# Optimization experiments

Hardware: AMD Instinct MI355X
Metric: run time of the kernel (lower is better)

Reference implementation:

```python
import jax, jax.numpy as jnp
import numpy as np

E, D_IN, H, D_OUT = 8, 6, 32, 2
B = 1048576

def setup_inputs() -> dict:
    key = jax.random.key(0)
    ks = jax.random.split(key, 11)
    s = lambda *sh: 1.0 / np.sqrt(sh[-2])  # glorot-ish scale
    x = jax.random.normal(ks[0], (B, D_IN), dtype=jnp.float32)
    # stacked expert weights
    W1 = jax.random.normal(ks[1], (E, D_IN, H), dtype=jnp.float32) * (1.0/np.sqrt(D_IN))
    b1 = jnp.zeros((E, H), dtype=jnp.float32)
    W2 = jax.random.normal(ks[2], (E, H, H), dtype=jnp.float32) * (1.0/np.sqrt(H))
    b2 = jnp.zeros((E, H), dtype=jnp.float32)
    W3 = jax.random.normal(ks[3], (E, H, D_OUT), dtype=jnp.float32) * (1.0/np.sqrt(H))
    b3 = jnp.zeros((E, D_OUT), dtype=jnp.float32)
    # gating network
    Wg1 = jax.random.normal(ks[4], (D_IN, H), dtype=jnp.float32) * (1.0/np.sqrt(D_IN))
    bg1 = jnp.zeros((H,), dtype=jnp.float32)
    Wg2 = jax.random.normal(ks[5], (H, E), dtype=jnp.float32) * (1.0/np.sqrt(H))
    bg2 = jnp.zeros((E,), dtype=jnp.float32)
    return {"x": x, "W1": W1, "b1": b1, "W2": W2, "b2": b2, "W3": W3, "b3": b3,
            "Wg1": Wg1, "bg1": bg1, "Wg2": Wg2, "bg2": bg2}

def reference(x, W1, b1, W2, b2, W3, b3, Wg1, bg1, Wg2, bg2):
    # gate: [B, E] softmax probs
    g = jax.nn.softmax(jax.nn.relu(x @ Wg1 + bg1) @ Wg2 + bg2, axis=-1)
    # all experts as batched GEMMs: h1, h2 [B, E, H]; y [B, E, 2]
    h1 = jax.nn.relu(jnp.einsum('bd,edh->beh', x, W1) + b1)
    h2 = jax.nn.relu(jnp.einsum('beh,ehk->bek', h1, W2) + b2)
    y = jnp.einsum('beh,eho->beo', h2, W3) + b3
    # gate-weighted sum over experts -> [B, 2]
    return jnp.einsum('be,beo->bo', g, y)
```

## Files before the change

kernel.cpp:

```cpp
#include <hip/hip_runtime.h>


typedef _Float16 half2_t __attribute__((ext_vector_type(2)));
typedef _Float16 half4_t __attribute__((ext_vector_type(4)));
typedef _Float16 half8_t __attribute__((ext_vector_type(8)));
typedef __fp16   fp16v2  __attribute__((ext_vector_type(2)));
typedef float  float4_t __attribute__((ext_vector_type(4)));
typedef float  float2_t __attribute__((ext_vector_type(2)));
typedef int    int2_t   __attribute__((ext_vector_type(2)));
typedef int    int4_t   __attribute__((ext_vector_type(4)));

#define MFMA_K32(A, B, C) __builtin_amdgcn_mfma_f32_16x16x32_f16((A), (B), (C), 0, 0, 0)
#define MFMA_K16(A, B, C) __builtin_amdgcn_mfma_f32_16x16x16f16((A), (B), (C), 0, 0, 0)

static constexpr int E_ = 8, DIN_ = 6, H_ = 32, EPW_ = 2;

union H8U { half2_t h2[4]; half8_t h8; int4_t i4; };
union H4U { half2_t h2[2]; half4_t h4; int2_t i2; };
union HI  { half2_t h; int i; };
union PKU { fp16v2 p; half2_t h; };
union FI  { float f; int i; };

__device__ __forceinline__ half2_t pkrtz(float a, float b) {
    PKU u; u.p = __builtin_amdgcn_cvt_pkrtz(a, b);
    return u.h;
}

__device__ __forceinline__ half2_t relu2(half2_t v) {
    const half2_t z = {(_Float16)0.0f, (_Float16)0.0f};
    return __builtin_elementwise_max(v, z);
}

__device__ __forceinline__ float bperm_f(int addr, float v) {
    FI u; u.f = v;
    u.i = __builtin_amdgcn_ds_bpermute(addr, u.i);
    return u.f;
}

__global__ __launch_bounds__(256, 2)
void moe_kernel(
    const float* __restrict__ x,  const float* __restrict__ W1, const float* __restrict__ b1,
    const float* __restrict__ W2, const float* __restrict__ b2, const float* __restrict__ W3,
    const float* __restrict__ b3, const float* __restrict__ Wg1, const float* __restrict__ bg1,
    const float* __restrict__ Wg2, const float* __restrict__ bg2,
    float* __restrict__ out, int nTiles, int tilesPerBlock)
{
    const int tid  = threadIdx.x;
    const int lane = tid & 63;
    const int t    = lane & 15;
    const int q    = lane >> 4;
    const int wv   = tid >> 6;
    const int eb   = wv * EPW_;

    __shared__ float2_t cbuf[2][4][16];

    const float L2E = 1.44269504f;

    H4U G1[2];
    #pragma unroll
    for (int f = 0; f < 2; ++f) {
        float v0 = 0.f, v1 = 0.f, v2 = 0.f, v3 = 0.f;
        if (q == 0) {
            v0 = Wg1[0 * H_ + f * 16 + t]; v1 = Wg1[1 * H_ + f * 16 + t];
            v2 = Wg1[2 * H_ + f * 16 + t]; v3 = Wg1[3 * H_ + f * 16 + t];
        } else if (q == 1) {
            v0 = Wg1[4 * H_ + f * 16 + t]; v1 = Wg1[5 * H_ + f * 16 + t];
            v2 = bg1[f * 16 + t];          v3 = 0.f;
        }
        G1[f].h2[0] = pkrtz(v0, v1); G1[f].h2[1] = pkrtz(v2, v3);
    }
    H8U G2;
    #pragma unroll
    for (int p = 0; p < 4; ++p) {
        int c0 = ((p >> 1) << 4) + q * 4 + ((p & 1) << 1);
        float v0 = (t < E_) ? Wg2[c0 * E_ + t] * L2E : 0.f;
        float v1 = (t < E_) ? Wg2[(c0 + 1) * E_ + t] * L2E : 0.f;
        G2.h2[p] = pkrtz(v0, v1);
    }

    H4U W1F[EPW_][2];
    H8U W2F[EPW_][2], W3F[EPW_], B2R[EPW_];
    #pragma unroll
    for (int j = 0; j < EPW_; ++j) {
        const int e = eb + j;
        #pragma unroll
        for (int f = 0; f < 2; ++f) {
            float v0 = 0.f, v1 = 0.f, v2 = 0.f, v3 = 0.f;
            const float* We = W1 + (size_t)e * DIN_ * H_ + f * 16 + t;
            if (q == 0)      { v0 = We[0 * H_]; v1 = We[1 * H_]; v2 = We[2 * H_]; v3 = We[3 * H_]; }
            else if (q == 1) { v0 = We[4 * H_]; v1 = We[5 * H_]; v2 = b1[e * H_ + f * 16 + t]; }
            W1F[j][f].h2[0] = pkrtz(v0, v1); W1F[j][f].h2[1] = pkrtz(v2, v3);
        }
        #pragma unroll
        for (int p = 0; p < 4; ++p) {
            int c0 = ((p >> 1) << 4) + q * 4 + ((p & 1) << 1);
            W2F[j][0].h2[p] = pkrtz(W2[(e * H_ + c0) * H_ + 0  + t], W2[(e * H_ + c0 + 1) * H_ + 0  + t]);
            W2F[j][1].h2[p] = pkrtz(W2[(e * H_ + c0) * H_ + 16 + t], W2[(e * H_ + c0 + 1) * H_ + 16 + t]);
            B2R[j].h2[p]    = pkrtz(b2[e * H_ + c0], b2[e * H_ + c0 + 1]);
            float v0 = 0.f, v1 = 0.f;
            if ((t >> 1) == e) {
                v0 = W3[(e * H_ + c0) * 2 + (t & 1)];
                v1 = W3[(e * H_ + c0 + 1) * 2 + (t & 1)];
            }
            W3F[j].h2[p] = pkrtz(v0, v1);
        }
    }

    float4_t bg2F, b3F;
    #pragma unroll
    for (int r = 0; r < 4; ++r) {
        int m = q * 4 + r;
        bg2F[r] = (m < E_) ? bg2[m] * L2E : 0.f;
        b3F[r]  = b3[m];
    }
    const float4_t zero4 = {0.f, 0.f, 0.f, 0.f};

    const int gsrc = ((((q >> 1) << 4) | t) << 2);
    const int csrc = (((wv << 4) | t) << 2);

    const int tile0 = blockIdx.x * tilesPerBlock;

    const int xo1 = (q == 0) ? 0 : 4;
    const int xo2 = (q == 0) ? 2 : 4;
    const float* xq = x + ((size_t)tile0 * 16 + t) * DIN_;
    float2_t la = {0.f, 0.f}, lb = {0.f, 0.f};
    if (tile0 < nTiles) {
        la = *(const float2_t*)(xq + xo1);
        lb = *(const float2_t*)(xq + xo2);
    }

    HI onei; onei.h = pkrtz(1.f, 0.f);
    const bool isq0 = (q == 0);

    for (int it = 0; it < tilesPerBlock; ++it) {
        const int tile = tile0 + it;
        if (tile >= nTiles) break;

        H4U ux;
        ux.h2[0] = pkrtz(la[0], la[1]);
        HI hb; hb.h = pkrtz(lb[0], lb[1]);
        HI se; se.i = isq0 ? hb.i : onei.i;
        ux.h2[1] = se.h;
        const half4_t xB = ux.h4;

        if ((it + 1) < tilesPerBlock && (tile + 1) < nTiles) {
            const float* xn = xq + (size_t)(it + 1) * 16 * DIN_;
            la = *(const float2_t*)(xn + xo1);
            lb = *(const float2_t*)(xn + xo2);
        }

        float4_t hgLo = MFMA_K16(G1[0].h4, xB, zero4);
        float4_t hgHi = MFMA_K16(G1[1].h4, xB, zero4);
        H8U uh;
        uh.h2[0] = relu2(pkrtz(hgLo[0], hgLo[1]));
        uh.h2[1] = relu2(pkrtz(hgLo[2], hgLo[3]));
        uh.h2[2] = relu2(pkrtz(hgHi[0], hgHi[1]));
        uh.h2[3] = relu2(pkrtz(hgHi[2], hgHi[3]));
        float4_t gl = MFMA_K32(G2.h8, uh.h8, bg2F);

        float ex0 = __builtin_amdgcn_exp2f(gl[0]);
        float ex1 = __builtin_amdgcn_exp2f(gl[1]);
        float ex2 = __builtin_amdgcn_exp2f(gl[2]);
        float ex3 = __builtin_amdgcn_exp2f(gl[3]);
        float s = (ex0 + ex1) + (ex2 + ex3);
        s += __shfl_xor(s, 16);
        float rs = __builtin_amdgcn_rcpf(s);
        HI pa, pb;
        pa.h = pkrtz(ex0, ex1);
        pb.h = pkrtz(ex2, ex3);
        int va = __builtin_amdgcn_ds_bpermute(gsrc, pa.i);
        int vb = __builtin_amdgcn_ds_bpermute(gsrc, pb.i);
        HI gsel; gsel.i = (q & 1) ? vb : va;
        float ga = (float)gsel.h[0];
        float gb = (float)gsel.h[1];

        float4_t Y = b3F;
        #pragma unroll
        for (int j = 0; j < EPW_; ++j) {
            float4_t lo = MFMA_K16(W1F[j][0].h4, xB, zero4);
            float4_t hi = MFMA_K16(W1F[j][1].h4, xB, zero4);
            H8U u1;
            u1.h2[0] = relu2(pkrtz(lo[0], lo[1]));
            u1.h2[1] = relu2(pkrtz(lo[2], lo[3]));
            u1.h2[2] = relu2(pkrtz(hi[0], hi[1]));
            u1.h2[3] = relu2(pkrtz(hi[2], hi[3]));
            float4_t lo2 = MFMA_K32(W2F[j][0].h8, u1.h8, zero4);
            float4_t hi2 = MFMA_K32(W2F[j][1].h8, u1.h8, zero4);
            H8U u2;
            u2.h2[0] = relu2(pkrtz(lo2[0], lo2[1]) + B2R[j].h2[0]);
            u2.h2[1] = relu2(pkrtz(lo2[2], lo2[3]) + B2R[j].h2[1]);
            u2.h2[2] = relu2(pkrtz(hi2[0], hi2[1]) + B2R[j].h2[2]);
            u2.h2[3] = relu2(pkrtz(hi2[2], hi2[3]) + B2R[j].h2[3]);
            Y = MFMA_K32(W3F[j].h8, u2.h8, Y);
        }

        float p0 = ga * Y[0] + gb * Y[2];
        float p1 = ga * Y[1] + gb * Y[3];
        p0 = bperm_f(csrc, p0);
        p1 = bperm_f(csrc, p1);

        if (lane < 16) {
            float2_t o = {p0, p1};
            cbuf[it & 1][wv][t] = o;
        }
        __syncthreads();
        if (wv == 0 && lane < 16) {
            float2_t o  = cbuf[it & 1][0][t];
            float2_t o1 = cbuf[it & 1][1][t];
            float2_t o2 = cbuf[it & 1][2][t];
            float2_t o3 = cbuf[it & 1][3][t];
            o[0] = (o[0] + o1[0] + o2[0] + o3[0]) * rs;
            o[1] = (o[1] + o1[1] + o2[1] + o3[1]) * rs;
            *(float2_t*)(out + ((size_t)tile * 16 + t) * 2) = o;
        }
    }
}

extern "C" void kernel_launch(void* const* d_in, const int* in_sizes, int n_in,
                              void* d_out, int out_size, void* d_ws, size_t ws_size,
                              hipStream_t stream) {
    const float* x   = (const float*)d_in[0];
    const float* W1  = (const float*)d_in[1];
    const float* b1  = (const float*)d_in[2];
    const float* W2  = (const float*)d_in[3];
    const float* b2  = (const float*)d_in[4];
    const float* W3  = (const float*)d_in[5];
    const float* b3  = (const float*)d_in[6];
    const float* Wg1 = (const float*)d_in[7];
    const float* bg1 = (const float*)d_in[8];
    const float* Wg2 = (const float*)d_in[9];
    const float* bg2 = (const float*)d_in[10];
    float* out = (float*)d_out;

    const int B      = in_sizes[0] / DIN_;
    const int nTiles = (B + 15) / 16;
    const int blocks = 2048;
    const int tpb    = (nTiles + blocks - 1) / blocks;

    moe_kernel<<<blocks, 256, 0, stream>>>(x, W1, b1, W2, b2, W3, b3,
                                           Wg1, bg1, Wg2, bg2, out, nTiles, tpb);
}
```

Measured before the change: 156.7 us.

## Assign all experts to each wave and drop cross-wave shared-memory reduction

Each wave now computes all eight experts for its own row tiles instead of four waves splitting experts on one tile. This removes the per-tile LDS write, block barrier and final cross-wave sum, and the gate network is no longer computed redundantly by every wave. The expert output accumulation is split into two accumulators to shorten the MFMA dependency chain, and the grid is reduced so each wave handles more tiles. The cost is far more weight fragments held in registers per thread and fewer total waves, which may reduce occupancy and latency hiding.

Result: slower. 177.3 us (+13.2%).

```diff
diff --git a/kernel.cpp b/kernel.cpp
--- a/kernel.cpp
+++ b/kernel.cpp
@@ -13,13 +13,12 @@
 #define MFMA_K32(A, B, C) __builtin_amdgcn_mfma_f32_16x16x32_f16((A), (B), (C), 0, 0, 0)
 #define MFMA_K16(A, B, C) __builtin_amdgcn_mfma_f32_16x16x16f16((A), (B), (C), 0, 0, 0)
 
-static constexpr int E_ = 8, DIN_ = 6, H_ = 32, EPW_ = 2;
+static constexpr int E_ = 8, DIN_ = 6, H_ = 32, EPW_ = 8;
 
 union H8U { half2_t h2[4]; half8_t h8; int4_t i4; };
 union H4U { half2_t h2[2]; half4_t h4; int2_t i2; };
 union HI  { half2_t h; int i; };
 union PKU { fp16v2 p; half2_t h; };
-union FI  { float f; int i; };
 
 __device__ __forceinline__ half2_t pkrtz(float a, float b) {
     PKU u; u.p = __builtin_amdgcn_cvt_pkrtz(a, b);
@@ -29,12 +28,6 @@
 __device__ __forceinline__ half2_t relu2(half2_t v) {
     const half2_t z = {(_Float16)0.0f, (_Float16)0.0f};
     return __builtin_elementwise_max(v, z);
-}
-
-__device__ __forceinline__ float bperm_f(int addr, float v) {
-    FI u; u.f = v;
-    u.i = __builtin_amdgcn_ds_bpermute(addr, u.i);
-    return u.f;
 }
 
 __global__ __launch_bounds__(256, 2)
@@ -43,16 +36,13 @@
     const float* __restrict__ W2, const float* __restrict__ b2, const float* __restrict__ W3,
     const float* __restrict__ b3, const float* __restrict__ Wg1, const float* __restrict__ bg1,
     const float* __restrict__ Wg2, const float* __restrict__ bg2,
-    float* __restrict__ out, int nTiles, int tilesPerBlock)
+    float* __restrict__ out, int nTiles, int tilesPerWave)
 {
     const int tid  = threadIdx.x;
     const int lane = tid & 63;
     const int t    = lane & 15;
     const int q    = lane >> 4;
-    const int wv   = tid >> 6;
-    const int eb   = wv * EPW_;
-
-    __shared__ float2_t cbuf[2][4][16];
+    const int gw   = (blockIdx.x << 2) + (tid >> 6);
 
     const float L2E = 1.44269504f;
 
@@ -81,28 +71,27 @@
     H4U W1F[EPW_][2];
     H8U W2F[EPW_][2], W3F[EPW_], B2R[EPW_];
     #pragma unroll
-    for (int j = 0; j < EPW_; ++j) {
-        const int e = eb + j;
+    for (int e = 0; e < EPW_; ++e) {
         #pragma unroll
         for (int f = 0; f < 2; ++f) {
             float v0 = 0.f, v1 = 0.f, v2 = 0.f, v3 = 0.f;
             const float* We = W1 + (size_t)e * DIN_ * H_ + f * 16 + t;
             if (q == 0)      { v0 = We[0 * H_]; v1 = We[1 * H_]; v2 = We[2 * H_]; v3 = We[3 * H_]; }
             else if (q == 1) { v0 = We[4 * H_]; v1 = We[5 * H_]; v2 = b1[e * H_ + f * 16 + t]; }
-            W1F[j][f].h2[0] = pkrtz(v0, v1); W1F[j][f].h2[1] = pkrtz(v2, v3);
+            W1F[e][f].h2[0] = pkrtz(v0, v1); W1F[e][f].h2[1] = pkrtz(v2, v3);
         }
         #pragma unroll
         for (int p = 0; p < 4; ++p) {
             int c0 = ((p >> 1) << 4) + q * 4 + ((p & 1) << 1);
-            W2F[j][0].h2[p] = pkrtz(W2[(e * H_ + c0) * H_ + 0  + t], W2[(e * H_ + c0 + 1) * H_ + 0  + t]);
-            W2F[j][1].h2[p] = pkrtz(W2[(e * H_ + c0) * H_ + 16 + t], W2[(e * H_ + c0 + 1) * H_ + 16 + t]);
-            B2R[j].h2[p]    = pkrtz(b2[e * H_ + c0], b2[e * H_ + c0 + 1]);
+            W2F[e][0].h2[p] = pkrtz(W2[(e * H_ + c0) * H_ + 0  + t], W2[(e * H_ + c0 + 1) * H_ + 0  + t]);
+            W2F[e][1].h2[p] = pkrtz(W2[(e * H_ + c0) * H_ + 16 + t], W2[(e * H_ + c0 + 1) * H_ + 16 + t]);
+            B2R[e].h2[p]    = pkrtz(b2[e * H_ + c0], b2[e * H_ + c0 + 1]);
             float v0 = 0.f, v1 = 0.f;
             if ((t >> 1) == e) {
                 v0 = W3[(e * H_ + c0) * 2 + (t & 1)];
                 v1 = W3[(e * H_ + c0 + 1) * 2 + (t & 1)];
             }
-            W3F[j].h2[p] = pkrtz(v0, v1);
+            W3F[e].h2[p] = pkrtz(v0, v1);
         }
     }
 
@@ -116,9 +105,8 @@
     const float4_t zero4 = {0.f, 0.f, 0.f, 0.f};
 
     const int gsrc = ((((q >> 1) << 4) | t) << 2);
-    const int csrc = (((wv << 4) | t) << 2);
-
-    const int tile0 = blockIdx.x * tilesPerBlock;
+
+    const int tile0 = gw * tilesPerWave;
 
     const int xo1 = (q == 0) ? 0 : 4;
     const int xo2 = (q == 0) ? 2 : 4;
@@ -132,7 +120,7 @@
     HI onei; onei.h = pkrtz(1.f, 0.f);
     const bool isq0 = (q == 0);
 
-    for (int it = 0; it < tilesPerBlock; ++it) {
+    for (int it = 0; it < tilesPerWave; ++it) {
         const int tile = tile0 + it;
         if (tile >= nTiles) break;
 
@@ -143,7 +131,7 @@
         ux.h2[1] = se.h;
         const half4_t xB = ux.h4;
 
-        if ((it + 1) < tilesPerBlock && (tile + 1) < nTiles) {
+        if ((it + 1) < tilesPerWave && (tile + 1) < nTiles) {
             const float* xn = xq + (size_t)(it + 1) * 16 * DIN_;
             la = *(const float2_t*)(xn + xo1);
             lb = *(const float2_t*)(xn + xo2);
@@ -174,43 +162,36 @@
         float ga = (float)gsel.h[0];
         float gb = (float)gsel.h[1];
 
-        float4_t Y = b3F;
+        float4_t Ya = b3F, Yb = zero4;
         #pragma unroll
-        for (int j = 0; j < EPW_; ++j) {
-            float4_t lo = MFMA_K16(W1F[j][0].h4, xB, zero4);
-            float4_t hi = MFMA_K16(W1F[j][1].h4, xB, zero4);
+        for (int e = 0; e < EPW_; ++e) {
+            float4_t lo = MFMA_K16(W1F[e][0].h4, xB, zero4);
+            float4_t hi = MFMA_K16(W1F[e][1].h4, xB, zero4);
             H8U u1;
             u1.h2[0] = relu2(pkrtz(lo[0], lo[1]));
             u1.h2[1] = relu2(pkrtz(lo[2], lo[3]));
             u1.h2[2] = relu2(pkrtz(hi[0], hi[1]));
             u1.h2[3] = relu2(pkrtz(hi[2], hi[3]));
-            float4_t lo2 = MFMA_K32(W2F[j][0].h8, u1.h8, zero4);
-            float4_t hi2 = MFMA_K32(W2F[j][1].h8, u1.h8, zero4);
+            float4_t lo2 = MFMA_K32(W2F[e][0].h8, u1.h8, zero4);
+            float4_t hi2 = MFMA_K32(W2F[e][1].h8, u1.h8, zero4);
             H8U u2;
-            u2.h2[0] = relu2(pkrtz(lo2[0], lo2[1]) + B2R[j].h2[0]);
-            u2.h2[1] = relu2(pkrtz(lo2[2], lo2[3]) + B2R[j].h2[1]);
-            u2.h2[2] = relu2(pkrtz(hi2[0], hi2[1]) + B2R[j].h2[2]);
-            u2.h2[3] = relu2(pkrtz(hi2[2], hi2[3]) + B2R[j].h2[3]);
-            Y = MFMA_K32(W3F[j].h8, u2.h8, Y);
-        }
-
-        float p0 = ga * Y[0] + gb * Y[2];
-        float p1 = ga * Y[1] + gb * Y[3];
-        p0 = bperm_f(csrc, p0);
-        p1 = bperm_f(csrc, p1);
+            u2.h2[0] = relu2(pkrtz(lo2[0], lo2[1]) + B2R[e].h2[0]);
+            u2.h2[1] = relu2(pkrtz(lo2[2], lo2[3]) + B2R[e].h2[1]);
+            u2.h2[2] = relu2(pkrtz(hi2[0], hi2[1]) + B2R[e].h2[2]);
+            u2.h2[3] = relu2(pkrtz(hi2[2], hi2[3]) + B2R[e].h2[3]);
+            if (e & 1) Yb = MFMA_K32(W3F[e].h8, u2.h8, Yb);
+            else       Ya = MFMA_K32(W3F[e].h8, u2.h8, Ya);
+        }
+
+        float p0 = ga * (Ya[0] + Yb[0]) + gb * (Ya[2] + Yb[2]);
+        float p1 = ga * (Ya[1] + Yb[1]) + gb * (Ya[3] + Yb[3]);
+        p0 += __shfl_xor(p0, 16);
+        p0 += __shfl_xor(p0, 32);
+        p1 += __shfl_xor(p1, 16);
+        p1 += __shfl_xor(p1, 32);
 
         if (lane < 16) {
-            float2_t o = {p0, p1};
-            cbuf[it & 1][wv][t] = o;
-        }
-        __syncthreads();
-        if (wv == 0 && lane < 16) {
-            float2_t o  = cbuf[it & 1][0][t];
-            float2_t o1 = cbuf[it & 1][1][t];
-            float2_t o2 = cbuf[it & 1][2][t];
-            float2_t o3 = cbuf[it & 1][3][t];
-            o[0] = (o[0] + o1[0] + o2[0] + o3[0]) * rs;
-            o[1] = (o[1] + o1[1] + o2[1] + o3[1]) * rs;
+            float2_t o = {p0 * rs, p1 * rs};
             *(float2_t*)(out + ((size_t)tile * 16 + t) * 2) = o;
         }
     }
@@ -234,9 +215,10 @@
 
     const int B      = in_sizes[0] / DIN_;
     const int nTiles = (B + 15) / 16;
-    const int blocks = 2048;
-    const int tpb    = (nTiles + blocks - 1) / blocks;
+    const int blocks = 512;
+    const int wavesTotal = blocks * 4;
+    const int tpw = (nTiles + wavesTotal - 1) / wavesTotal;
 
     moe_kernel<<<blocks, 256, 0, stream>>>(x, W1, b1, W2, b2, W3, b3,
-                                           Wg1, bg1, Wg2, bg2, out, nTiles, tpb);
-}
+                                           Wg1, bg1, Wg2, bg2, out, nTiles, tpw);
+}
```
